# Performance work log

Hardware: AMD Instinct MI355X
Metric: run time of the kernel (lower is better)

Reference implementation:

```python
import jax, jax.numpy as jnp
import numpy as np

TAU = 0.2
EPS = 1e-12  # matches torch F.normalize eps


def _l2_normalize(x):
    # F.normalize(x, p=2, dim=1): x / max(||x||, eps)
    norm = jnp.sqrt(jnp.sum(x * x, axis=1, keepdims=True))
    return x / jnp.maximum(norm, EPS)


def setup_inputs() -> dict:
    key = jax.random.key(0)
    k1, k2 = jax.random.split(key)
    N, D = 16384, 256
    z1 = jax.random.normal(k1, (N, D), dtype=jnp.float32)
    z2 = jax.random.normal(k2, (N, D), dtype=jnp.float32)
    return {"z1": z1, "z2": z2}


def reference(z1, z2):
    # semi_loss: f(x) = exp(x / tau) over full cosine-similarity matrix
    h1 = _l2_normalize(z1)
    h2 = _l2_normalize(z2)
    sim = jnp.einsum('nd,md->nm', h1, h2)          # [N, N] cosine similarities
    between = jnp.exp(sim / TAU)                   # f(pair_sim)
    diag = jnp.diagonal(between)                   # positive pairs
    row_sum = jnp.sum(between, axis=1)
    loss = jnp.sum(-jnp.log(diag / (row_sum - diag)))
    return loss
```

## Files before the change

### kernel.cpp

```cpp
#include <hip/hip_runtime.h>
#include <hip/hip_bf16.h>

#define NROWS 16384
#define DDIM  256
#define LOG2E 1.4426950408889634f
#define SCALE 7.213475204444817f

typedef __attribute__((ext_vector_type(4))) float f32x4;
typedef __attribute__((ext_vector_type(2))) float f32x2;
typedef __attribute__((ext_vector_type(4))) int   i32x4;
typedef __attribute__((ext_vector_type(8))) int   i32x8;

#define UNIT_SCALE 0x7F7F7F7F

__global__ __launch_bounds__(256) void prep_kernel(
    const float* __restrict__ z1, const float* __restrict__ z2,
    unsigned char* __restrict__ h1q, unsigned char* __restrict__ h2t,
    float* __restrict__ diag5, float* __restrict__ rowsum) {
  int tid = threadIdx.x;
  int w = tid >> 6, lane = tid & 63;
  int r = blockIdx.x * 4 + w;

  const float4 a = ((const float4*)z1)[r * 64 + lane];
  const float4 b = ((const float4*)z2)[r * 64 + lane];

  float ss1 = a.x * a.x + a.y * a.y + a.z * a.z + a.w * a.w;
  float ss2 = b.x * b.x + b.y * b.y + b.z * b.z + b.w * b.w;
  float dp  = a.x * b.x + a.y * b.y + a.z * b.z + a.w * b.w;
  #pragma unroll
  for (int m = 1; m <= 32; m <<= 1) {
    ss1 += __shfl_xor(ss1, m);
    ss2 += __shfl_xor(ss2, m);
    dp  += __shfl_xor(dp, m);
  }
  float inv1 = 1.0f / fmaxf(sqrtf(ss1), 1e-12f);
  float inv2 = 1.0f / fmaxf(sqrtf(ss2), 1e-12f);
  float s1 = inv1 * SCALE;

  int p1 = __builtin_amdgcn_cvt_pk_fp8_f32(a.x * s1, a.y * s1, 0, false);
  p1     = __builtin_amdgcn_cvt_pk_fp8_f32(a.z * s1, a.w * s1, p1, true);
  int p2 = __builtin_amdgcn_cvt_pk_fp8_f32(b.x * inv2, b.y * inv2, 0, false);
  p2     = __builtin_amdgcn_cvt_pk_fp8_f32(b.z * inv2, b.w * inv2, p2, true);
  ((int*)h1q)[r * 64 + lane] = p1;

  {
    int c = lane >> 2, sub = lane & 3;
    int off = (r >> 4) * 4096 + (c >> 3) * 2048 + (c & 1) * 1024 +
              ((c >> 1) & 3) * 256 + (r & 15) * 16 + sub * 4;
    *(int*)(h2t + off) = p2;
  }

  if (lane == 0) diag5[r] = dp * inv1 * inv2 * 5.0f;
  if (tid < 4) rowsum[blockIdx.x * 4 + tid] = 0.0f;
}

#define CSPL 8

#define LOADSET(B, P0, P1) do { \
  B[0] = *reinterpret_cast<const i32x4*>(P0); \
  B[1] = *reinterpret_cast<const i32x4*>(P0 + 1024); \
  B[2] = *reinterpret_cast<const i32x4*>(P0 + 2048); \
  B[3] = *reinterpret_cast<const i32x4*>(P0 + 3072); \
  B[4] = *reinterpret_cast<const i32x4*>(P1); \
  B[5] = *reinterpret_cast<const i32x4*>(P1 + 1024); \
  B[6] = *reinterpret_cast<const i32x4*>(P1 + 2048); \
  B[7] = *reinterpret_cast<const i32x4*>(P1 + 3072); \
  P0 += 8192; P1 += 8192; } while (0)

#define MFMA_S(Aop, Bop, Cop) \
  __builtin_amdgcn_mfma_scale_f32_16x16x128_f8f6f4( \
      Aop, Bop, Cop, 0, 0, 0, UNIT_SCALE, 0, UNIT_SCALE)

#define COMPUTE(B) do { \
  union { i32x8 v; i32x4 h[2]; } u00, u01, u10, u11; \
  u00.h[0] = B[0]; u00.h[1] = B[1]; u01.h[0] = B[2]; u01.h[1] = B[3]; \
  u10.h[0] = B[4]; u10.h[1] = B[5]; u11.h[0] = B[6]; u11.h[1] = B[7]; \
  f32x4 a0[4], a1[4]; \
  _Pragma("unroll") for (int m = 0; m < 4; ++m) a0[m] = MFMA_S(afr[m][0], u00.v, ZV); \
  _Pragma("unroll") for (int m = 0; m < 4; ++m) a1[m] = MFMA_S(afr[m][0], u10.v, ZV); \
  _Pragma("unroll") for (int m = 0; m < 4; ++m) a0[m] = MFMA_S(afr[m][1], u01.v, a0[m]); \
  _Pragma("unroll") for (int m = 0; m < 4; ++m) a1[m] = MFMA_S(afr[m][1], u11.v, a1[m]); \
  _Pragma("unroll") for (int m = 0; m < 4; ++m) { \
    rs2[m][0] += (f32x2){__builtin_amdgcn_exp2f(a0[m][0]), __builtin_amdgcn_exp2f(a0[m][1])}; \
    rs2[m][1] += (f32x2){__builtin_amdgcn_exp2f(a0[m][2]), __builtin_amdgcn_exp2f(a0[m][3])}; \
    rs2[m][0] += (f32x2){__builtin_amdgcn_exp2f(a1[m][0]), __builtin_amdgcn_exp2f(a1[m][1])}; \
    rs2[m][1] += (f32x2){__builtin_amdgcn_exp2f(a1[m][2]), __builtin_amdgcn_exp2f(a1[m][3])}; \
  } } while (0)

__global__ __launch_bounds__(256) void simexp_kernel(
    const unsigned char* __restrict__ h1q, const unsigned char* __restrict__ h2t,
    float* __restrict__ rowsum) {
  int tid = threadIdx.x, w = tid >> 6, lane = tid & 63;
  int bx = blockIdx.x;
  int rb = bx >> 3;
  int cs = bx & 7;
  int row0 = rb * 256 + w * 64;

  const char* h1b = (const char*)h1q;

  i32x8 afr[4][2];
  #pragma unroll
  for (int m = 0; m < 4; ++m)
    #pragma unroll
    for (int ks = 0; ks < 2; ++ks) {
      int row = row0 + m * 16 + (lane & 15);
      int off = row * 256 + ks * 128 + (lane >> 4) * 32;
      afr[m][ks] = *reinterpret_cast<const i32x8*>(h1b + off);
    }
  #pragma unroll
  for (int m = 0; m < 4; ++m)
    #pragma unroll
    for (int ks = 0; ks < 2; ++ks)
      asm volatile("" : "+v"(afr[m][ks]));

  const char* Bp0 = (const char*)h2t + (size_t)cs * 524288 + lane * 16;
  const char* Bp1 = Bp0 + 4096;

  const f32x4 ZV = {0.f, 0.f, 0.f, 0.f};
  f32x2 rs2[4][2];
  #pragma unroll
  for (int m = 0; m < 4; ++m) {
    rs2[m][0] = (f32x2){0.f, 0.f};
    rs2[m][1] = (f32x2){0.f, 0.f};
  }

  i32x4 bufA[8], bufB[8];
  LOADSET(bufA, Bp0, Bp1);

  for (int jt2 = 0; jt2 < 32; ++jt2) {
    LOADSET(bufB, Bp0, Bp1);
    COMPUTE(bufA);
    LOADSET(bufA, Bp0, Bp1);
    COMPUTE(bufB);
  }

  #pragma unroll
  for (int m = 0; m < 4; ++m)
    #pragma unroll
    for (int p = 0; p < 2; ++p)
      #pragma unroll
      for (int c = 0; c < 2; ++c) {
        float v = rs2[m][p][c];
        v += __shfl_xor(v, 1);
        v += __shfl_xor(v, 2);
        v += __shfl_xor(v, 4);
        v += __shfl_xor(v, 8);
        if ((lane & 15) == 0)
          atomicAdd(&rowsum[row0 + m * 16 + (lane >> 4) * 4 + p * 2 + c], v);
      }
}

__global__ __launch_bounds__(1024) void loss_kernel(
    const float* __restrict__ rowsum, const float* __restrict__ diag5,
    float* __restrict__ out) {
  int tid = threadIdx.x;
  float s = 0.0f;
  for (int i = tid; i < NROWS; i += 1024) {
    float d5 = diag5[i];
    float de = __builtin_amdgcn_exp2f(d5 * LOG2E);
    s += logf(rowsum[i] - de) - d5;
  }
  #pragma unroll
  for (int m = 1; m <= 32; m <<= 1) s += __shfl_xor(s, m);
  __shared__ float wsum[16];
  if ((tid & 63) == 0) wsum[tid >> 6] = s;
  __syncthreads();
  if (tid == 0) {
    float t = 0.0f;
    #pragma unroll
    for (int i = 0; i < 16; ++i) t += wsum[i];
    out[0] = t;
  }
}

extern "C" void kernel_launch(void* const* d_in, const int* in_sizes, int n_in,
                              void* d_out, int out_size, void* d_ws, size_t ws_size,
                              hipStream_t stream) {
  const float* z1 = (const float*)d_in[0];
  const float* z2 = (const float*)d_in[1];

  char* ws = (char*)d_ws;
  unsigned char* h1q = (unsigned char*)(ws);
  unsigned char* h2t = (unsigned char*)(ws + 4194304);
  float* diag5 = (float*)(ws + 8421376);
  float* rowsm = (float*)(ws + 8486912);
  if (ws_size < 8552448) return;

  prep_kernel<<<4096, 256, 0, stream>>>(z1, z2, h1q, h2t, diag5, rowsm);
  simexp_kernel<<<512, 256, 0, stream>>>(h1q, h2t, rowsm);
  loss_kernel<<<1, 1024, 0, stream>>>(rowsm, diag5, (float*)d_out);
}
```

Baseline: 88.37 us.

## Split simexp into MFMA producer and exp consumer warps via LDS ping-pong

Each block now has 8 waves: 4 producer waves run the FP8 MFMAs and write accumulator tiles to a double-buffered 64KB LDS region, and 4 consumer waves read them and apply exp2 plus the row-sum accumulation. Producers get raised priority, and the two roles are stepped together with one __syncthreads per phase. The aim is to run the transcendental exp work on different waves from the matrix cores so the two overlap. In exchange it adds LDS write and read traffic, a barrier every phase, and lower occupancy from the 64KB of shared memory per block.

Result: slower. 93.66 us (+6.0%).

```diff
diff --git a/kernel.cpp b/kernel.cpp
--- a/kernel.cpp
+++ b/kernel.cpp
@@ -55,99 +55,118 @@
 }
 
 #define CSPL 8
-
-#define LOADSET(B, P0, P1) do { \
-  B[0] = *reinterpret_cast<const i32x4*>(P0); \
-  B[1] = *reinterpret_cast<const i32x4*>(P0 + 1024); \
-  B[2] = *reinterpret_cast<const i32x4*>(P0 + 2048); \
-  B[3] = *reinterpret_cast<const i32x4*>(P0 + 3072); \
-  B[4] = *reinterpret_cast<const i32x4*>(P1); \
-  B[5] = *reinterpret_cast<const i32x4*>(P1 + 1024); \
-  B[6] = *reinterpret_cast<const i32x4*>(P1 + 2048); \
-  B[7] = *reinterpret_cast<const i32x4*>(P1 + 3072); \
-  P0 += 8192; P1 += 8192; } while (0)
+#define NPH  64
 
 #define MFMA_S(Aop, Bop, Cop) \
   __builtin_amdgcn_mfma_scale_f32_16x16x128_f8f6f4( \
       Aop, Bop, Cop, 0, 0, 0, UNIT_SCALE, 0, UNIT_SCALE)
 
-#define COMPUTE(B) do { \
-  union { i32x8 v; i32x4 h[2]; } u00, u01, u10, u11; \
-  u00.h[0] = B[0]; u00.h[1] = B[1]; u01.h[0] = B[2]; u01.h[1] = B[3]; \
-  u10.h[0] = B[4]; u10.h[1] = B[5]; u11.h[0] = B[6]; u11.h[1] = B[7]; \
-  f32x4 a0[4], a1[4]; \
-  _Pragma("unroll") for (int m = 0; m < 4; ++m) a0[m] = MFMA_S(afr[m][0], u00.v, ZV); \
-  _Pragma("unroll") for (int m = 0; m < 4; ++m) a1[m] = MFMA_S(afr[m][0], u10.v, ZV); \
-  _Pragma("unroll") for (int m = 0; m < 4; ++m) a0[m] = MFMA_S(afr[m][1], u01.v, a0[m]); \
-  _Pragma("unroll") for (int m = 0; m < 4; ++m) a1[m] = MFMA_S(afr[m][1], u11.v, a1[m]); \
+#define PPHASE(T) do { \
+  const char* b_ = Bp + (T) * 8192; \
+  i32x4 B0 = *(const i32x4*)(b_); \
+  i32x4 B1 = *(const i32x4*)(b_ + 1024); \
+  i32x4 B2 = *(const i32x4*)(b_ + 2048); \
+  i32x4 B3 = *(const i32x4*)(b_ + 3072); \
+  union { i32x8 v; i32x4 h[2]; } u0_, u1_; \
+  u0_.h[0] = B0; u0_.h[1] = B1; u1_.h[0] = B2; u1_.h[1] = B3; \
+  f32x4 a_[4]; \
+  _Pragma("unroll") for (int m = 0; m < 4; ++m) a_[m] = MFMA_S(afr[m][0], u0_.v, ZV); \
+  _Pragma("unroll") for (int m = 0; m < 4; ++m) a_[m] = MFMA_S(afr[m][1], u1_.v, a_[m]); \
+  i32x4 B4 = *(const i32x4*)(b_ + 4096); \
+  i32x4 B5 = *(const i32x4*)(b_ + 5120); \
+  i32x4 B6 = *(const i32x4*)(b_ + 6144); \
+  i32x4 B7 = *(const i32x4*)(b_ + 7168); \
+  char* s_ = Sw + (((T) & 1) << 15); \
+  _Pragma("unroll") for (int m = 0; m < 4; ++m) *(f32x4*)(s_ + m * 1024) = a_[m]; \
+  u0_.h[0] = B4; u0_.h[1] = B5; u1_.h[0] = B6; u1_.h[1] = B7; \
+  _Pragma("unroll") for (int m = 0; m < 4; ++m) a_[m] = MFMA_S(afr[m][0], u0_.v, ZV); \
+  _Pragma("unroll") for (int m = 0; m < 4; ++m) a_[m] = MFMA_S(afr[m][1], u1_.v, a_[m]); \
+  _Pragma("unroll") for (int m = 0; m < 4; ++m) *(f32x4*)(s_ + 4096 + m * 1024) = a_[m]; \
+} while (0)
+
+#define CPHASE(T) do { \
+  const char* s_ = Sw + (((T) & 1) << 15); \
   _Pragma("unroll") for (int m = 0; m < 4; ++m) { \
-    rs2[m][0] += (f32x2){__builtin_amdgcn_exp2f(a0[m][0]), __builtin_amdgcn_exp2f(a0[m][1])}; \
-    rs2[m][1] += (f32x2){__builtin_amdgcn_exp2f(a0[m][2]), __builtin_amdgcn_exp2f(a0[m][3])}; \
-    rs2[m][0] += (f32x2){__builtin_amdgcn_exp2f(a1[m][0]), __builtin_amdgcn_exp2f(a1[m][1])}; \
-    rs2[m][1] += (f32x2){__builtin_amdgcn_exp2f(a1[m][2]), __builtin_amdgcn_exp2f(a1[m][3])}; \
-  } } while (0)
-
-__global__ __launch_bounds__(256) void simexp_kernel(
+    f32x4 v0 = *(const f32x4*)(s_ + m * 1024); \
+    f32x4 v1 = *(const f32x4*)(s_ + 4096 + m * 1024); \
+    rs2[m][0] += (f32x2){__builtin_amdgcn_exp2f(v0[0]), __builtin_amdgcn_exp2f(v0[1])}; \
+    rs2[m][1] += (f32x2){__builtin_amdgcn_exp2f(v0[2]), __builtin_amdgcn_exp2f(v0[3])}; \
+    rs2[m][0] += (f32x2){__builtin_amdgcn_exp2f(v1[0]), __builtin_amdgcn_exp2f(v1[1])}; \
+    rs2[m][1] += (f32x2){__builtin_amdgcn_exp2f(v1[2]), __builtin_amdgcn_exp2f(v1[3])}; \
+  } \
+} while (0)
+
+__global__ __launch_bounds__(512) void simexp_kernel(
     const unsigned char* __restrict__ h1q, const unsigned char* __restrict__ h2t,
     float* __restrict__ rowsum) {
+  __shared__ alignas(16) unsigned char sacc[2][32768];
+
   int tid = threadIdx.x, w = tid >> 6, lane = tid & 63;
   int bx = blockIdx.x;
   int rb = bx >> 3;
   int cs = bx & 7;
-  int row0 = rb * 256 + w * 64;
-
-  const char* h1b = (const char*)h1q;
-
+  bool prod = (w < 4);
+  int p = prod ? w : (w - 4);
+  int row0 = rb * 256 + p * 64;
+
+  const char* Bp = (const char*)h2t + (size_t)cs * 524288 + lane * 16;
+  char* Sw = (char*)&sacc[0][0] + p * 8192 + lane * 16;
+
+  const f32x4 ZV = {0.f, 0.f, 0.f, 0.f};
   i32x8 afr[4][2];
-  #pragma unroll
-  for (int m = 0; m < 4; ++m)
-    #pragma unroll
-    for (int ks = 0; ks < 2; ++ks) {
-      int row = row0 + m * 16 + (lane & 15);
-      int off = row * 256 + ks * 128 + (lane >> 4) * 32;
-      afr[m][ks] = *reinterpret_cast<const i32x8*>(h1b + off);
+  f32x2 rs2[4][2];
+
+  if (prod) {
+    const char* h1b = (const char*)h1q;
+    #pragma unroll
+    for (int m = 0; m < 4; ++m)
+      #pragma unroll
+      for (int ks = 0; ks < 2; ++ks) {
+        int row = row0 + m * 16 + (lane & 15);
+        afr[m][ks] = *reinterpret_cast<const i32x8*>(
+            h1b + row * 256 + ks * 128 + (lane >> 4) * 32);
+      }
+    #pragma unroll
+    for (int m = 0; m < 4; ++m)
+      #pragma unroll
+      for (int ks = 0; ks < 2; ++ks)
+        asm volatile("" : "+v"(afr[m][ks]));
+    __builtin_amdgcn_s_setprio(1);
+  } else {
+    #pragma unroll
+    for (int m = 0; m < 4; ++m) {
+      rs2[m][0] = (f32x2){0.f, 0.f};
+      rs2[m][1] = (f32x2){0.f, 0.f};
     }
-  #pragma unroll
-  for (int m = 0; m < 4; ++m)
-    #pragma unroll
-    for (int ks = 0; ks < 2; ++ks)
-      asm volatile("" : "+v"(afr[m][ks]));
-
-  const char* Bp0 = (const char*)h2t + (size_t)cs * 524288 + lane * 16;
-  const char* Bp1 = Bp0 + 4096;
-
-  const f32x4 ZV = {0.f, 0.f, 0.f, 0.f};
-  f32x2 rs2[4][2];
-  #pragma unroll
-  for (int m = 0; m < 4; ++m) {
-    rs2[m][0] = (f32x2){0.f, 0.f};
-    rs2[m][1] = (f32x2){0.f, 0.f};
-  }
-
-  i32x4 bufA[8], bufB[8];
-  LOADSET(bufA, Bp0, Bp1);
-
-  for (int jt2 = 0; jt2 < 32; ++jt2) {
-    LOADSET(bufB, Bp0, Bp1);
-    COMPUTE(bufA);
-    LOADSET(bufA, Bp0, Bp1);
-    COMPUTE(bufB);
-  }
-
-  #pragma unroll
-  for (int m = 0; m < 4; ++m)
-    #pragma unroll
-    for (int p = 0; p < 2; ++p)
+  }
+
+  if (prod) PPHASE(0);
+  __syncthreads();
+
+  #pragma unroll 2
+  for (int t = 1; t < NPH; ++t) {
+    if (prod) PPHASE(t);
+    else      CPHASE(t - 1);
+    __syncthreads();
+  }
+
+  if (!prod) {
+    CPHASE(NPH - 1);
+    #pragma unroll
+    for (int m = 0; m < 4; ++m)
       #pragma unroll
-      for (int c = 0; c < 2; ++c) {
-        float v = rs2[m][p][c];
-        v += __shfl_xor(v, 1);
-        v += __shfl_xor(v, 2);
-        v += __shfl_xor(v, 4);
-        v += __shfl_xor(v, 8);
-        if ((lane & 15) == 0)
-          atomicAdd(&rowsum[row0 + m * 16 + (lane >> 4) * 4 + p * 2 + c], v);
-      }
+      for (int q = 0; q < 2; ++q)
+        #pragma unroll
+        for (int c = 0; c < 2; ++c) {
+          float v = rs2[m][q][c];
+          v += __shfl_xor(v, 1);
+          v += __shfl_xor(v, 2);
+          v += __shfl_xor(v, 4);
+          v += __shfl_xor(v, 8);
+          if ((lane & 15) == 0)
+            atomicAdd(&rowsum[row0 + m * 16 + (lane >> 4) * 4 + q * 2 + c], v);
+        }
+  }
 }
 
 __global__ __launch_bounds__(1024) void loss_kernel(
@@ -187,6 +206,6 @@
   if (ws_size < 8552448) return;
 
   prep_kernel<<<4096, 256, 0, stream>>>(z1, z2, h1q, h2t, diag5, rowsm);
-  simexp_kernel<<<512, 256, 0, stream>>>(h1q, h2t, rowsm);
+  simexp_kernel<<<512, 512, 0, stream>>>(h1q, h2t, rowsm);
   loss_kernel<<<1, 1024, 0, stream>>>(rowsm, diag5, (float*)d_out);
 }
```
